# Kernel optimization log

Hardware: AMD Instinct MI355X
Metric: run time of the kernel (lower is better)

Reference implementation:

```python
import jax, jax.numpy as jnp
import numpy as np

D_MODEL = 1024
N_HEADS = 16
HEAD_DIM = D_MODEL // N_HEADS
B, T = 2, 2048

def setup_inputs() -> dict:
    key = jax.random.key(0)
    ks = jax.random.split(key, 9)
    s = 1.0 / np.sqrt(D_MODEL)
    return {
        "x": jax.random.normal(ks[0], (B, T, D_MODEL), dtype=jnp.float32),
        "Wq": jax.random.normal(ks[1], (D_MODEL, D_MODEL), dtype=jnp.float32) * s,
        "bq": jax.random.normal(ks[2], (D_MODEL,), dtype=jnp.float32) * 0.01,
        "Wk": jax.random.normal(ks[3], (D_MODEL, D_MODEL), dtype=jnp.float32) * s,
        "bk": jax.random.normal(ks[4], (D_MODEL,), dtype=jnp.float32) * 0.01,
        "Wv": jax.random.normal(ks[5], (D_MODEL, D_MODEL), dtype=jnp.float32) * s,
        "bv": jax.random.normal(ks[6], (D_MODEL,), dtype=jnp.float32) * 0.01,
        "Wo": jax.random.normal(ks[7], (D_MODEL, D_MODEL), dtype=jnp.float32) * s,
        "bo": jax.random.normal(ks[8], (D_MODEL,), dtype=jnp.float32) * 0.01,
    }

def reference(x, Wq, bq, Wk, bk, Wv, bv, Wo, bo):
    b, t, c = x.shape
    # Projections; reshape to [B, H, T, Dh]
    def heads(w, bias):
        return (x @ w.T + bias).reshape(b, t, N_HEADS, HEAD_DIM).transpose(0, 2, 1, 3)
    q = heads(Wq, bq)
    k = heads(Wk, bk)
    v = heads(Wv, bv)
    scale = 1.0 / np.sqrt(HEAD_DIM)
    att = jnp.einsum("bhqd,bhkd->bhqk", q, k) * scale  # [B,H,T,T]
    causal = jnp.tril(jnp.ones((t, t), dtype=bool))
    att = jnp.where(causal, att, -jnp.inf)
    att = jax.nn.softmax(att, axis=-1)
    # dropout p=0.0 (eval) -> identity
    y = jnp.einsum("bhqk,bhkd->bhqd", att, v)  # [B,H,T,Dh]
    y = y.transpose(0, 2, 1, 3).reshape(b, t, c)
    return y @ Wo.T + bo
```

## Files before the change

### kernel.cpp

```cpp
#include <hip/hip_runtime.h>
#include <stdint.h>


typedef unsigned short u16;
typedef __attribute__((ext_vector_type(8)))  __bf16 bf16x8;
typedef __attribute__((ext_vector_type(4)))  float  f32x4;
typedef __attribute__((ext_vector_type(16))) float  f32x16;
typedef __attribute__((ext_vector_type(4)))  float  float4v;
typedef __attribute__((ext_vector_type(4)))  unsigned short u16x4;
typedef __attribute__((ext_vector_type(4)))  unsigned int   u32x4;
typedef __attribute__((ext_vector_type(8)))  short  short8;

#define BB 2
#define TT 2048
#define DD 1024
#define HH 16
#define DH 64
#define MM (BB*TT)
#define NSLOT 1280
#define CEXP 0.18033688011f
#define XNE ((size_t)MM*DD)
#define WNE ((size_t)DD*DD)

static __device__ __forceinline__ u16 f2bf(float f) {
    uint32_t u = __builtin_bit_cast(uint32_t, f);
    u += 0x7FFFu + ((u >> 16) & 1u);
    return (u16)(u >> 16);
}
static __device__ __forceinline__ float bf2f(u16 v) {
    uint32_t u = (uint32_t)v << 16;
    return __builtin_bit_cast(float, u);
}

static __device__ __forceinline__ unsigned cvt_pk_bf16(float a, float b) {
    unsigned r;
    asm("v_cvt_pk_bf16_f32 %0, %1, %2" : "=v"(r) : "v"(a), "v"(b));
    return r;
}

static __device__ __forceinline__ void load_lds16(const u16* g, const u16* lds_base) {
    __builtin_amdgcn_global_load_lds(
        (const __attribute__((address_space(1))) void*)(uintptr_t)g,
        (__attribute__((address_space(3)))  void*)(uint32_t)(uintptr_t)lds_base,
        16u, 0, 0u);
}

static __device__ __forceinline__ f32x4 mfma16(bf16x8 a, bf16x8 b, f32x4 c) {
    return __builtin_amdgcn_mfma_f32_16x16x32_bf16(a, b, c, 0, 0, 0);
}
static __device__ __forceinline__ f32x16 mfma32(bf16x8 a, bf16x8 b, f32x16 c) {
    return __builtin_amdgcn_mfma_f32_32x32x16_bf16(a, b, c, 0, 0, 0);
}

static __device__ __forceinline__ float tree_sum16(const f32x16& a) {
    float m[8];
#pragma unroll
    for (int r = 0; r < 8; ++r) m[r] = a[r] + a[r + 8];
#pragma unroll
    for (int off = 4; off; off >>= 1)
#pragma unroll
        for (int r = 0; r < off; ++r) m[r] += m[r + off];
    return m[0];
}

static __device__ __forceinline__ bf16x8 pack8(float s0, float s1, float s2,
        float s3, float s4, float s5, float s6, float s7) {
    unsigned c0 = cvt_pk_bf16(s0, s1);
    unsigned c1 = cvt_pk_bf16(s2, s3);
    unsigned c2 = cvt_pk_bf16(s4, s5);
    unsigned c3 = cvt_pk_bf16(s6, s7);
    asm volatile("v_permlane32_swap_b32 %0, %1" : "+v"(c0), "+v"(c2));
    asm volatile("v_permlane32_swap_b32 %0, %1" : "+v"(c1), "+v"(c3));
    u32x4 w; w[0] = c0; w[1] = c1; w[2] = c2; w[3] = c3;
    return __builtin_bit_cast(bf16x8, w);
}

__global__ __launch_bounds__(256) void cvt_kernel(const float* __restrict__ src,
                                                  u16* __restrict__ dst, int n4) {
    int i = blockIdx.x * blockDim.x + threadIdx.x;
    int stride = gridDim.x * blockDim.x;
    for (; i < n4; i += stride) {
        float4v v = ((const float4v*)src)[i];
        u16x4 o;
        o[0] = f2bf(v[0]); o[1] = f2bf(v[1]); o[2] = f2bf(v[2]); o[3] = f2bf(v[3]);
        ((u16x4*)dst)[i] = o;
    }
}

__global__ __launch_bounds__(256) void cvt4_kernel(const float* __restrict__ s0,
        const float* __restrict__ s1, const float* __restrict__ s2,
        const float* __restrict__ s3, u16* __restrict__ d0, u16* __restrict__ d1,
        u16* __restrict__ d2, u16* __restrict__ d3, int n4) {
    const int z = blockIdx.y;
    const float* src = (z == 0) ? s0 : (z == 1) ? s1 : (z == 2) ? s2 : s3;
    u16* dst = (z == 0) ? d0 : (z == 1) ? d1 : (z == 2) ? d2 : d3;
    const float sc = (z == 0) ? CEXP : 1.0f;
    int i = blockIdx.x * blockDim.x + threadIdx.x;
    int stride = gridDim.x * blockDim.x;
    for (; i < n4; i += stride) {
        float4v v = ((const float4v*)src)[i];
        u16x4 o;
        o[0] = f2bf(v[0] * sc); o[1] = f2bf(v[1] * sc);
        o[2] = f2bf(v[2] * sc); o[3] = f2bf(v[3] * sc);
        ((u16x4*)dst)[i] = o;
    }
}

template<int MODE>
__global__ __launch_bounds__(256) void gemm2(const u16* __restrict__ xb,
        const u16* __restrict__ Wb, const float* __restrict__ bq,
        const float* __restrict__ bk, const float* __restrict__ bvv,
        u16* __restrict__ outq, u16* __restrict__ vt, float* __restrict__ outf) {
    __shared__ alignas(16) u16 As[2][128 * 32];
    __shared__ alignas(16) u16 Bs[2][128 * 32];

    const int tid  = threadIdx.x;
    const int wave = tid >> 6, lane = tid & 63;
    const int lr = lane & 15, lg = lane >> 4;
    const int wr = wave >> 1, wc = wave & 1;
    const int K = 1024;

    const u16 *Ap, *Wp;
    int m0, n0, zb = 0;
    bool vtmode = false;
    const int id = blockIdx.x;
    if (MODE == 0) {
        if (id < 512) {
            zb = id >> 8; int r = id & 255;
            m0 = (r >> 3) * 128; n0 = (r & 7) * 128;
            Ap = xb; Wp = Wb + (size_t)zb * WNE;
        } else {
            int v = id - 512; zb = v >> 7; int r = v & 127;
            m0 = (r >> 4) * 128; n0 = (r & 15) * 128;
            Ap = Wb + 2 * WNE;
            Wp = xb + (size_t)zb * 2048 * 1024;
            vtmode = true;
        }
    } else {
        m0 = (id >> 3) * 128; n0 = (id & 7) * 128;
        Ap = xb; Wp = Wb;
    }

    f32x4 acc[4][4];
#pragma unroll
    for (int m = 0; m < 4; ++m)
#pragma unroll
        for (int n = 0; n < 4; ++n) acc[m][n] = (f32x4){0.f, 0.f, 0.f, 0.f};

#define G_STAGE(BB_, KK_)                                                     \
    {                                                                         \
        _Pragma("unroll")                                                     \
        for (int it = 0; it < 2; ++it) {                                      \
            int c = it * 256 + tid;                                           \
            int row = c >> 2, cc = (c & 3) * 8;                               \
            load_lds16(Ap + (size_t)(m0 + row) * K + (KK_) + cc,              \
                       &As[BB_][(size_t)(it * 256 + wave * 64) * 8]);         \
            load_lds16(Wp + (size_t)(n0 + row) * K + (KK_) + cc,              \
                       &Bs[BB_][(size_t)(it * 256 + wave * 64) * 8]);         \
        }                                                                     \
    }

    G_STAGE(0, 0);
    __syncthreads();
    int cur = 0;
    for (int k0 = 0; k0 < K; k0 += 32) {
        if (k0 + 32 < K) G_STAGE(cur ^ 1, k0 + 32);

        bf16x8 af[4], bfm[4];
#pragma unroll
        for (int m = 0; m < 4; ++m)
            af[m] = *(const bf16x8*)&As[cur][(wr * 64 + m * 16 + lr) * 32 + lg * 8];
#pragma unroll
        for (int n = 0; n < 4; ++n)
            bfm[n] = *(const bf16x8*)&Bs[cur][(wc * 64 + n * 16 + lr) * 32 + lg * 8];
#pragma unroll
        for (int m = 0; m < 4; ++m)
#pragma unroll
            for (int n = 0; n < 4; ++n)
                acc[m][n] = mfma16(af[m], bfm[n], acc[m][n]);

        __syncthreads();
        cur ^= 1;
    }
#undef G_STAGE

    if (MODE == 1) {
#pragma unroll
        for (int n = 0; n < 4; ++n) {
            int col = n0 + wc * 64 + n * 16 + lr;
            float bvl = bq[col];
#pragma unroll
            for (int m = 0; m < 4; ++m) {
                int row = m0 + wr * 64 + m * 16 + lg * 4;
#pragma unroll
                for (int r = 0; r < 4; ++r)
                    outf[(size_t)(row + r) * 1024 + col] = acc[m][n][r] + bvl;
            }
        }
    } else if (!vtmode) {
        const float* bias = zb ? bk : bq;
        const float bsc = zb ? 1.0f : CEXP;
#pragma unroll
        for (int n = 0; n < 4; ++n) {
            int col = n0 + wc * 64 + n * 16 + lr;
            float bvl = bias[col] * bsc;
#pragma unroll
            for (int m = 0; m < 4; ++m) {
                int row = m0 + wr * 64 + m * 16 + lg * 4;
#pragma unroll
                for (int r = 0; r < 4; ++r)
                    outq[(size_t)zb * XNE + (size_t)(row + r) * 1024 + col] =
                        f2bf(acc[m][n][r] + bvl);
            }
        }
    } else {
        u16* vo = vt + (size_t)zb * 1024 * 2048;
#pragma unroll
        for (int m = 0; m < 4; ++m) {
            int rowb = m0 + wr * 64 + m * 16 + lg * 4;
            float bvr[4];
#pragma unroll
            for (int r = 0; r < 4; ++r) bvr[r] = bvv[rowb + r];
#pragma unroll
            for (int n = 0; n < 4; ++n) {
                int col = n0 + wc * 64 + n * 16 + lr;
#pragma unroll
                for (int r = 0; r < 4; ++r)
                    vo[(size_t)(rowb + r) * 2048 + col] = f2bf(acc[m][n][r] + bvr[r]);
            }
        }
    }
}

__global__ __launch_bounds__(256) void attn_part(const u16* __restrict__ Qb,
        const u16* __restrict__ Kb, const u16* __restrict__ VTb,
        u16* __restrict__ Op, float* __restrict__ Ml, u16* __restrict__ Yb) {
    __shared__ alignas(16) u16 Ks[2][64 * 64];
    __shared__ alignas(16) u16 Vs[2][64 * 64];

    const int tid  = threadIdx.x;
    const int wave = tid >> 6, lane = tid & 63;
    const int lq = lane & 31, hi = lane >> 5;

    const int i0 = blockIdx.x;
    const int bh = (i0 & 7) * 4 + ((i0 >> 3) / 40);
    const int s  = (i0 >> 3) % 40;
    int qi = 0, ch = 0;
    {
        int cum = 0, found = 0;
#pragma unroll
        for (int j = 0; j < 16; ++j) {
            int n = (j >> 2) + 1;
            if (!found && s < cum + n) { qi = j; ch = s - cum; found = 1; }
            cum += n;
        }
    }
    const int nc = (qi >> 2) + 1;
    const int b = bh >> 4, h = bh & 15;
    const size_t rb = (size_t)b * TT;
    const int hoff = h * DH;
    const int q0w = qi * 128 + wave * 32;
    const int k0 = ch * 512;
    const int kend = qi * 128 + 128;
    const int k1 = (k0 + 512 < kend) ? k0 + 512 : kend;

    const int srow0 = tid >> 3, sl = tid & 7;
    const int srow1 = (256 + tid) >> 3;

    const u16* Kbh = Kb + rb * DD + hoff;
    const u16* Vbh = VTb + (size_t)bh * 64 * 2048;

    bf16x8 qf[4];
    {
        const u16* qrow = Qb + (rb + q0w + lq) * DD + hoff + hi * 8;
#pragma unroll
        for (int kc = 0; kc < 4; ++kc) qf[kc] = *(const bf16x8*)(qrow + kc * 16);
    }

    f32x16 o0 = {}, o1 = {};
    float l_i = 0.f;

#define A_STAGE(BB_, KV_)                                                     \
    {                                                                         \
        load_lds16(Kbh + (size_t)((KV_) + srow0) * DD + (sl ^ (srow0 & 7)) * 8,\
                   &Ks[BB_][(size_t)(wave * 64) * 8]);                        \
        load_lds16(Kbh + (size_t)((KV_) + srow1) * DD + (sl ^ (srow1 & 7)) * 8,\
                   &Ks[BB_][(size_t)(256 + wave * 64) * 8]);                  \
        load_lds16(Vbh + (size_t)srow0 * 2048 + (KV_) + (sl ^ (srow0 & 7)) * 8,\
                   &Vs[BB_][(size_t)(wave * 64) * 8]);                        \
        load_lds16(Vbh + (size_t)srow1 * 2048 + (KV_) + (sl ^ (srow1 & 7)) * 8,\
                   &Vs[BB_][(size_t)(256 + wave * 64) * 8]);                  \
    }

    A_STAGE(0, k0);
    __syncthreads();
    int cur = 0;

    for (int kv0 = k0; kv0 < k1; kv0 += 64) {
        if (kv0 + 64 < k1) A_STAGE(cur ^ 1, kv0 + 64);

        if (kv0 < q0w + 32) {
            const int rowm = lq & 7;
            const bool diag = (kv0 + 63 > q0w);
            const int qrel = q0w + lq - kv0;
            bf16x8 pb[4];

            {
                f32x16 st = {};
                __builtin_amdgcn_s_setprio(1);
#pragma unroll
                for (int kc = 0; kc < 4; ++kc) {
                    bf16x8 kf = *(const bf16x8*)&Ks[cur][lq * 64 + ((2 * kc + hi) ^ rowm) * 8];
                    st = mfma32(kf, qf[kc], st);
                }
                __builtin_amdgcn_s_setprio(0);
                if (diag) {
#pragma unroll
                    for (int r = 0; r < 16; ++r) {
                        int key = (r & 3) + 8 * (r >> 2) + 4 * hi;
                        if (key > qrel) st[r] = -1e30f;
                    }
                }
#pragma unroll
                for (int r = 0; r < 16; ++r) st[r] = __builtin_amdgcn_exp2f(st[r]);
                l_i += tree_sum16(st);
                pb[0] = pack8(st[0], st[1], st[2], st[3], st[4], st[5], st[6], st[7]);
                pb[1] = pack8(st[8], st[9], st[10], st[11], st[12], st[13], st[14], st[15]);
            }
            {
                f32x16 st = {};
                __builtin_amdgcn_s_setprio(1);
#pragma unroll
                for (int kc = 0; kc < 4; ++kc) {
                    bf16x8 kf = *(const bf16x8*)&Ks[cur][(32 + lq) * 64 + ((2 * kc + hi) ^ rowm) * 8];
                    st = mfma32(kf, qf[kc], st);
                }
                __builtin_amdgcn_s_setprio(0);
                if (diag) {
#pragma unroll
                    for (int r = 0; r < 16; ++r) {
                        int key = 32 + (r & 3) + 8 * (r >> 2) + 4 * hi;
                        if (key > qrel) st[r] = -1e30f;
                    }
                }
#pragma unroll
                for (int r = 0; r < 16; ++r) st[r] = __builtin_amdgcn_exp2f(st[r]);
                l_i += tree_sum16(st);
                pb[2] = pack8(st[0], st[1], st[2], st[3], st[4], st[5], st[6], st[7]);
                pb[3] = pack8(st[8], st[9], st[10], st[11], st[12], st[13], st[14], st[15]);
            }

            __builtin_amdgcn_s_setprio(1);
#pragma unroll
            for (int ks = 0; ks < 4; ++ks) {
                bf16x8 vf0 = *(const bf16x8*)&Vs[cur][lq * 64        + ((ks * 2 + hi) ^ rowm) * 8];
                bf16x8 vf1 = *(const bf16x8*)&Vs[cur][(32 + lq) * 64 + ((ks * 2 + hi) ^ rowm) * 8];
                o0 = mfma32(vf0, pb[ks], o0);
                o1 = mfma32(vf1, pb[ks], o1);
            }
            __builtin_amdgcn_s_setprio(0);
        }

        __syncthreads();
        cur ^= 1;
    }
#undef A_STAGE

    l_i += __shfl_xor(l_i, 32);
    const int col = wave * 32 + lq;

    if (nc == 1) {
        const float inv = 1.0f / l_i;
        u16* yrow = Yb + (rb + q0w + lq) * DD + hoff;
#pragma unroll
        for (int g = 0; g < 4; ++g) {
            u16x4 p0, p1;
#pragma unroll
            for (int j = 0; j < 4; ++j) {
                p0[j] = f2bf(o0[4 * g + j] * inv);
                p1[j] = f2bf(o1[4 * g + j] * inv);
            }
            *(u16x4*)&yrow[8 * g + 4 * hi]      = p0;
            *(u16x4*)&yrow[32 + 8 * g + 4 * hi] = p1;
        }
    } else {
        const int slot = bh * 40 + s;
        u16* op = Op + (size_t)slot * 8192;
#pragma unroll
        for (int r = 0; r < 16; ++r) {
            const int d0 = (r & 3) + 8 * (r >> 2) + 4 * hi;
            op[d0 * 128 + col]        = f2bf(o0[r]);
            op[(32 + d0) * 128 + col] = f2bf(o1[r]);
        }
        if (hi == 0) Ml[(size_t)slot * 128 + col] = l_i;
    }
}

__global__ __launch_bounds__(256) void attn_merge(const u16* __restrict__ Op,
        const float* __restrict__ Ml, u16* __restrict__ Yb) {
    const int bq = blockIdx.x;
    const int bh = bq >> 4, qi = bq & 15;
    const int nc = (qi >> 2) + 1;
    if (nc == 1) return;
    int cum = 0;
#pragma unroll
    for (int j = 0; j < 16; ++j) cum += (j < qi) ? ((j >> 2) + 1) : 0;
    const int s0 = bh * 40 + cum;

    const int t = threadIdx.x;
    const int row = t >> 1, dh = (t & 1) * 32;

    float L = 0.f;
    float acc[32];
#pragma unroll
    for (int d = 0; d < 32; ++d) acc[d] = 0.f;
#pragma unroll
    for (int c = 0; c < 4; ++c) {
        if (c < nc) {
            L += Ml[(size_t)(s0 + c) * 128 + row];
            const u16* op = Op + (size_t)(s0 + c) * 8192 + row;
#pragma unroll
            for (int d = 0; d < 32; ++d)
                acc[d] += bf2f(op[(dh + d) * 128]);
        }
    }
    const float inv = 1.0f / L;

    const int b = bh >> 4, h = bh & 15;
    u16* yrow = Yb + ((size_t)(b * TT + qi * 128 + row)) * DD + h * DH + dh;
#pragma unroll
    for (int g = 0; g < 8; ++g) {
        u16x4 p;
#pragma unroll
        for (int j = 0; j < 4; ++j) p[j] = f2bf(acc[4 * g + j] * inv);
        *(u16x4*)&yrow[4 * g] = p;
    }
}

extern "C" void kernel_launch(void* const* d_in, const int* in_sizes, int n_in,
                              void* d_out, int out_size, void* d_ws, size_t ws_size,
                              hipStream_t stream) {
    const float* x  = (const float*)d_in[0];
    const float* Wq = (const float*)d_in[1];
    const float* bq = (const float*)d_in[2];
    const float* Wk = (const float*)d_in[3];
    const float* bk = (const float*)d_in[4];
    const float* Wv = (const float*)d_in[5];
    const float* bv = (const float*)d_in[6];
    const float* Wo = (const float*)d_in[7];
    const float* bo = (const float*)d_in[8];
    float* out = (float*)d_out;

    u16* xb  = (u16*)d_ws;
    u16* Wb  = xb  + XNE;
    u16* Wob = Wb  + 3 * WNE;
    u16* QKV = Wob + WNE;
    u16* Yb  = QKV + 3 * XNE;
    u16* Op  = Yb  + XNE;
    float* Ml = (float*)(Op + (size_t)NSLOT * 8192);

    cvt_kernel<<<2048, 256, 0, stream>>>(x, xb, (int)(XNE / 4));
    cvt4_kernel<<<dim3(256, 4), 256, 0, stream>>>(Wq, Wk, Wv, Wo,
            Wb, Wb + WNE, Wb + 2 * WNE, Wob, (int)(WNE / 4));

    gemm2<0><<<768, 256, 0, stream>>>(xb, Wb, bq, bk, bv,
                                      QKV, QKV + 2 * XNE, nullptr);
    attn_part<<<NSLOT, 256, 0, stream>>>(QKV, QKV + XNE, QKV + 2 * XNE,
                                         Op, Ml, Yb);
    attn_merge<<<512, 256, 0, stream>>>(Op, Ml, Yb);
    gemm2<1><<<256, 256, 0, stream>>>(Yb, Wob, bo, nullptr, nullptr,
                                      nullptr, nullptr, out);
}
```

Measured before the change: 120.3 us.

## Split causal attention into smaller KV chunks, single-buffer LDS, widen cvt kernels

The attention split-K chunk shrinks from 512 to 256 keys, growing the slot count from 1280 to 2304 blocks, and the merge kernel now combines up to 8 partials. The aim is better load balance and occupancy across CUs. K/V LDS staging drops double buffering for a single buffer with two barriers per step. That halves shared memory but gives up load/compute overlap. The float-to-bf16 conversion kernels now handle 8 elements per thread using the packed convert instruction.

```diff
diff --git a/kernel.cpp b/kernel.cpp
--- a/kernel.cpp
+++ b/kernel.cpp
@@ -17,7 +17,7 @@
 #define HH 16
 #define DH 64
 #define MM (BB*TT)
-#define NSLOT 1280
+#define NSLOT 2304
 #define CEXP 0.18033688011f
 #define XNE ((size_t)MM*DD)
 #define WNE ((size_t)DD*DD)
@@ -76,33 +76,38 @@
 }
 
 __global__ __launch_bounds__(256) void cvt_kernel(const float* __restrict__ src,
-                                                  u16* __restrict__ dst, int n4) {
+                                                  u16* __restrict__ dst, int n8) {
     int i = blockIdx.x * blockDim.x + threadIdx.x;
     int stride = gridDim.x * blockDim.x;
-    for (; i < n4; i += stride) {
-        float4v v = ((const float4v*)src)[i];
-        u16x4 o;
-        o[0] = f2bf(v[0]); o[1] = f2bf(v[1]); o[2] = f2bf(v[2]); o[3] = f2bf(v[3]);
-        ((u16x4*)dst)[i] = o;
+    for (; i < n8; i += stride) {
+        float4v a = ((const float4v*)src)[2 * i];
+        float4v b = ((const float4v*)src)[2 * i + 1];
+        u32x4 o;
+        o[0] = cvt_pk_bf16(a[0], a[1]); o[1] = cvt_pk_bf16(a[2], a[3]);
+        o[2] = cvt_pk_bf16(b[0], b[1]); o[3] = cvt_pk_bf16(b[2], b[3]);
+        ((u32x4*)dst)[i] = o;
     }
 }
 
 __global__ __launch_bounds__(256) void cvt4_kernel(const float* __restrict__ s0,
         const float* __restrict__ s1, const float* __restrict__ s2,
         const float* __restrict__ s3, u16* __restrict__ d0, u16* __restrict__ d1,
-        u16* __restrict__ d2, u16* __restrict__ d3, int n4) {
+        u16* __restrict__ d2, u16* __restrict__ d3, int n8) {
     const int z = blockIdx.y;
     const float* src = (z == 0) ? s0 : (z == 1) ? s1 : (z == 2) ? s2 : s3;
     u16* dst = (z == 0) ? d0 : (z == 1) ? d1 : (z == 2) ? d2 : d3;
     const float sc = (z == 0) ? CEXP : 1.0f;
     int i = blockIdx.x * blockDim.x + threadIdx.x;
     int stride = gridDim.x * blockDim.x;
-    for (; i < n4; i += stride) {
-        float4v v = ((const float4v*)src)[i];
-        u16x4 o;
-        o[0] = f2bf(v[0] * sc); o[1] = f2bf(v[1] * sc);
-        o[2] = f2bf(v[2] * sc); o[3] = f2bf(v[3] * sc);
-        ((u16x4*)dst)[i] = o;
+    for (; i < n8; i += stride) {
+        float4v a = ((const float4v*)src)[2 * i];
+        float4v b = ((const float4v*)src)[2 * i + 1];
+        u32x4 o;
+        o[0] = cvt_pk_bf16(a[0] * sc, a[1] * sc);
+        o[1] = cvt_pk_bf16(a[2] * sc, a[3] * sc);
+        o[2] = cvt_pk_bf16(b[0] * sc, b[1] * sc);
+        o[3] = cvt_pk_bf16(b[2] * sc, b[3] * sc);
+        ((u32x4*)dst)[i] = o;
     }
 }
 
@@ -235,34 +240,34 @@
 __global__ __launch_bounds__(256) void attn_part(const u16* __restrict__ Qb,
         const u16* __restrict__ Kb, const u16* __restrict__ VTb,
         u16* __restrict__ Op, float* __restrict__ Ml, u16* __restrict__ Yb) {
-    __shared__ alignas(16) u16 Ks[2][64 * 64];
-    __shared__ alignas(16) u16 Vs[2][64 * 64];
+    __shared__ alignas(16) u16 Ks[64 * 64];
+    __shared__ alignas(16) u16 Vs[64 * 64];
 
     const int tid  = threadIdx.x;
     const int wave = tid >> 6, lane = tid & 63;
     const int lq = lane & 31, hi = lane >> 5;
 
     const int i0 = blockIdx.x;
-    const int bh = (i0 & 7) * 4 + ((i0 >> 3) / 40);
-    const int s  = (i0 >> 3) % 40;
+    const int bh = (i0 & 7) * 4 + ((i0 >> 3) / 72);
+    const int s  = (i0 >> 3) % 72;
     int qi = 0, ch = 0;
     {
         int cum = 0, found = 0;
 #pragma unroll
         for (int j = 0; j < 16; ++j) {
-            int n = (j >> 2) + 1;
+            int n = (j + 2) >> 1;
             if (!found && s < cum + n) { qi = j; ch = s - cum; found = 1; }
             cum += n;
         }
     }
-    const int nc = (qi >> 2) + 1;
+    const int nc = (qi + 2) >> 1;
     const int b = bh >> 4, h = bh & 15;
     const size_t rb = (size_t)b * TT;
     const int hoff = h * DH;
     const int q0w = qi * 128 + wave * 32;
-    const int k0 = ch * 512;
+    const int k0 = ch * 256;
     const int kend = qi * 128 + 128;
-    const int k1 = (k0 + 512 < kend) ? k0 + 512 : kend;
+    const int k1 = (k0 + 256 < kend) ? k0 + 256 : kend;
 
     const int srow0 = tid >> 3, sl = tid & 7;
     const int srow1 = (256 + tid) >> 3;
@@ -280,24 +285,17 @@
     f32x16 o0 = {}, o1 = {};
     float l_i = 0.f;
 
-#define A_STAGE(BB_, KV_)                                                     \
-    {                                                                         \
-        load_lds16(Kbh + (size_t)((KV_) + srow0) * DD + (sl ^ (srow0 & 7)) * 8,\
-                   &Ks[BB_][(size_t)(wave * 64) * 8]);                        \
-        load_lds16(Kbh + (size_t)((KV_) + srow1) * DD + (sl ^ (srow1 & 7)) * 8,\
-                   &Ks[BB_][(size_t)(256 + wave * 64) * 8]);                  \
-        load_lds16(Vbh + (size_t)srow0 * 2048 + (KV_) + (sl ^ (srow0 & 7)) * 8,\
-                   &Vs[BB_][(size_t)(wave * 64) * 8]);                        \
-        load_lds16(Vbh + (size_t)srow1 * 2048 + (KV_) + (sl ^ (srow1 & 7)) * 8,\
-                   &Vs[BB_][(size_t)(256 + wave * 64) * 8]);                  \
-    }
-
-    A_STAGE(0, k0);
-    __syncthreads();
-    int cur = 0;
-
     for (int kv0 = k0; kv0 < k1; kv0 += 64) {
-        if (kv0 + 64 < k1) A_STAGE(cur ^ 1, kv0 + 64);
+        __syncthreads();
+        load_lds16(Kbh + (size_t)(kv0 + srow0) * DD + (sl ^ (srow0 & 7)) * 8,
+                   &Ks[(size_t)(wave * 64) * 8]);
+        load_lds16(Kbh + (size_t)(kv0 + srow1) * DD + (sl ^ (srow1 & 7)) * 8,
+                   &Ks[(size_t)(256 + wave * 64) * 8]);
+        load_lds16(Vbh + (size_t)srow0 * 2048 + kv0 + (sl ^ (srow0 & 7)) * 8,
+                   &Vs[(size_t)(wave * 64) * 8]);
+        load_lds16(Vbh + (size_t)srow1 * 2048 + kv0 + (sl ^ (srow1 & 7)) * 8,
+                   &Vs[(size_t)(256 + wave * 64) * 8]);
+        __syncthreads();
 
         if (kv0 < q0w + 32) {
             const int rowm = lq & 7;
@@ -310,7 +308,7 @@
                 __builtin_amdgcn_s_setprio(1);
 #pragma unroll
                 for (int kc = 0; kc < 4; ++kc) {
-                    bf16x8 kf = *(const bf16x8*)&Ks[cur][lq * 64 + ((2 * kc + hi) ^ rowm) * 8];
+                    bf16x8 kf = *(const bf16x8*)&Ks[lq * 64 + ((2 * kc + hi) ^ rowm) * 8];
                     st = mfma32(kf, qf[kc], st);
                 }
                 __builtin_amdgcn_s_setprio(0);
@@ -332,7 +330,7 @@
                 __builtin_amdgcn_s_setprio(1);
 #pragma unroll
                 for (int kc = 0; kc < 4; ++kc) {
-                    bf16x8 kf = *(const bf16x8*)&Ks[cur][(32 + lq) * 64 + ((2 * kc + hi) ^ rowm) * 8];
+                    bf16x8 kf = *(const bf16x8*)&Ks[(32 + lq) * 64 + ((2 * kc + hi) ^ rowm) * 8];
                     st = mfma32(kf, qf[kc], st);
                 }
                 __builtin_amdgcn_s_setprio(0);
@@ -353,18 +351,14 @@
             __builtin_amdgcn_s_setprio(1);
 #pragma unroll
             for (int ks = 0; ks < 4; ++ks) {
-                bf16x8 vf0 = *(const bf16x8*)&Vs[cur][lq * 64        + ((ks * 2 + hi) ^ rowm) * 8];
-                bf16x8 vf1 = *(const bf16x8*)&Vs[cur][(32 + lq) * 64 + ((ks * 2 + hi) ^ rowm) * 8];
+                bf16x8 vf0 = *(const bf16x8*)&Vs[lq * 64        + ((ks * 2 + hi) ^ rowm) * 8];
+                bf16x8 vf1 = *(const bf16x8*)&Vs[(32 + lq) * 64 + ((ks * 2 + hi) ^ rowm) * 8];
                 o0 = mfma32(vf0, pb[ks], o0);
                 o1 = mfma32(vf1, pb[ks], o1);
             }
             __builtin_amdgcn_s_setprio(0);
         }
-
-        __syncthreads();
-        cur ^= 1;
-    }
-#undef A_STAGE
+    }
 
     l_i += __shfl_xor(l_i, 32);
     const int col = wave * 32 + lq;
@@ -384,7 +378,7 @@
             *(u16x4*)&yrow[32 + 8 * g + 4 * hi] = p1;
         }
     } else {
-        const int slot = bh * 40 + s;
+        const int slot = bh * 72 + s;
         u16* op = Op + (size_t)slot * 8192;
 #pragma unroll
         for (int r = 0; r < 16; ++r) {
@@ -400,12 +394,12 @@
         const float* __restrict__ Ml, u16* __restrict__ Yb) {
     const int bq = blockIdx.x;
     const int bh = bq >> 4, qi = bq & 15;
-    const int nc = (qi >> 2) + 1;
+    const int nc = (qi + 2) >> 1;
     if (nc == 1) return;
     int cum = 0;
 #pragma unroll
-    for (int j = 0; j < 16; ++j) cum += (j < qi) ? ((j >> 2) + 1) : 0;
-    const int s0 = bh * 40 + cum;
+    for (int j = 0; j < 16; ++j) cum += (j < qi) ? ((j + 2) >> 1) : 0;
+    const int s0 = bh * 72 + cum;
 
     const int t = threadIdx.x;
     const int row = t >> 1, dh = (t & 1) * 32;
@@ -415,7 +409,7 @@
 #pragma unroll
     for (int d = 0; d < 32; ++d) acc[d] = 0.f;
 #pragma unroll
-    for (int c = 0; c < 4; ++c) {
+    for (int c = 0; c < 8; ++c) {
         if (c < nc) {
             L += Ml[(size_t)(s0 + c) * 128 + row];
             const u16* op = Op + (size_t)(s0 + c) * 8192 + row;
@@ -459,9 +453,9 @@
     u16* Op  = Yb  + XNE;
     float* Ml = (float*)(Op + (size_t)NSLOT * 8192);
 
-    cvt_kernel<<<2048, 256, 0, stream>>>(x, xb, (int)(XNE / 4));
-    cvt4_kernel<<<dim3(256, 4), 256, 0, stream>>>(Wq, Wk, Wv, Wo,
-            Wb, Wb + WNE, Wb + 2 * WNE, Wob, (int)(WNE / 4));
+    cvt_kernel<<<1024, 256, 0, stream>>>(x, xb, (int)(XNE / 8));
+    cvt4_kernel<<<dim3(128, 4), 256, 0, stream>>>(Wq, Wk, Wv, Wo,
+            Wb, Wb + WNE, Wb + 2 * WNE, Wob, (int)(WNE / 8));
 
     gemm2<0><<<768, 256, 0, stream>>>(xb, Wb, bq, bk, bv,
                                       QKV, QKV + 2 * XNE, nullptr);
```

After: 128.0 us. +6.5%, slower.
